# Kernel tuning notes

Measured on AMD Instinct MI355X. Metric: run time of the kernel, lower is better.

The kernel has to match this reference:

```python
import jax, jax.numpy as jnp
import numpy as np


def _dir_loss(sim, mask_f, ms):
    # sim: [N1, N2] similarities; mask_f: [N1, N2] float 0/1 positives; ms: [N1] float row-selection.
    # Row i contributes sum_{p in pos(i), n in neg(i)} -logsigmoid(sim[i,p] - sim[i,n])
    # = sum_{p,n} mp[i,p]*mn[i,n]*softplus(sim[i,n] - sim[i,p]).
    mp = mask_f * ms[:, None]           # [N1, N2] positive weights (zero for unselected rows)
    mn = (1.0 - mask_f) * ms[:, None]   # [N1, N2] negative weights
    # term[i, p, n] = softplus(sim[i, n] - sim[i, p]) = -logsigmoid(sim[i, p] - sim[i, n])
    term = jax.nn.softplus(sim[:, None, :] - sim[:, :, None])  # [N1, N2, N2]
    loss = jnp.sum(mp[:, :, None] * mn[:, None, :] * term)
    pair_num = jnp.sum(mp.sum(axis=1) * mn.sum(axis=1))
    return loss, pair_num


def setup_inputs() -> dict:
    key = jax.random.key(0)
    k1, k2, k3, k4, k5 = jax.random.split(key, 5)
    N1, N2, D = 512, 512, 1024
    return {
        "features1": jax.random.normal(k1, (N1, D), dtype=jnp.float32),
        "features2": jax.random.normal(k2, (N2, D), dtype=jnp.float32),
        "mask": jax.random.randint(k3, (N1, N2), 0, 2, dtype=jnp.int32),
        "mask_sents1": jax.random.randint(k4, (N1,), 0, 2).astype(jnp.bool_),
        "mask_sents2": jax.random.randint(k5, (N2,), 0, 2).astype(jnp.bool_),
    }


def reference(features1, features2, mask, mask_sents1, mask_sents2):
    # sim_type == 'dot' (default): raw dot-product similarity, no normalization,
    # and temperature is never applied in the original forward.
    dt = features1.dtype
    mask_f = mask.astype(dt)
    ms1 = mask_sents1.astype(dt)
    ms2 = mask_sents2.astype(dt)
    sim = features1 @ features2.T  # [N1, N2]
    loss1, pn1 = _dir_loss(sim, mask_f, ms1)
    loss2, pn2 = _dir_loss(sim.T, mask_f.T, ms2)
    loss = loss1 + loss2
    pair_num = pn1 + pn2
    return jnp.where(pair_num > 0, loss / pair_num, loss)
```

## Files before the change

kernel.cpp:

```cpp
#include <hip/hip_runtime.h>

#define NN 512
#define DD 1024

typedef __attribute__((ext_vector_type(8))) short short8;
typedef __attribute__((ext_vector_type(4))) float f32x4;

__device__ __forceinline__ float fast_exp2(float x) {
#if __has_builtin(__builtin_amdgcn_exp2f)
  return __builtin_amdgcn_exp2f(x);
#else
  return __expf(x * 0.6931471805599453f);
#endif
}
__device__ __forceinline__ float fast_log2(float x) {
#if __has_builtin(__builtin_amdgcn_logf)
  return __builtin_amdgcn_logf(x);
#else
  return __logf(x) * 1.4426950408889634f;
#endif
}

__device__ __forceinline__ void cvt2(float f0, float f1, unsigned& hi, unsigned& lo) {
  const unsigned u0 = __float_as_uint(f0), u1 = __float_as_uint(f1);
  const unsigned h0 = u0 & 0xFFFF0000u, h1 = u1 & 0xFFFF0000u;
  const float r0 = f0 - __uint_as_float(h0);
  const float r1 = f1 - __uint_as_float(h1);
  hi = (u0 >> 16) | h1;
  lo = (__float_as_uint(r0) >> 16) | (__float_as_uint(r1) & 0xFFFF0000u);
}

__device__ __forceinline__ void store8(unsigned short* hp, unsigned short* lp,
                                       float4 f0, float4 f1) {
  uint4 hi, lo;
  cvt2(f0.x, f0.y, hi.x, lo.x);
  cvt2(f0.z, f0.w, hi.y, lo.y);
  cvt2(f1.x, f1.y, hi.z, lo.z);
  cvt2(f1.z, f1.w, hi.w, lo.w);
  *(uint4*)hp = hi;
  *(uint4*)lp = lo;
}

__global__ __launch_bounds__(256) void gemm_kernel(const float* __restrict__ A,
                                                   const float* __restrict__ B,
                                                   float* __restrict__ simP,
                                                   float* __restrict__ simTP,
                                                   int ks) {
  __shared__ unsigned short Ah[64][40];
  __shared__ unsigned short Al[64][40];
  __shared__ unsigned short Bh[64][40];
  __shared__ unsigned short Bl[64][40];
  const int t = threadIdx.x;
  const int lane = t & 63;
  const int w = t >> 6;
  const int wm = w >> 1, wn = w & 1;
  const int row0 = blockIdx.y * 64, col0 = blockIdx.x * 64;
  const int z = blockIdx.z;
  const int kspan = DD / ks;
  const int kbeg = z * kspan;
  const int srow = t >> 2;
  const int skq = (t & 3) << 3;

  f32x4 acc[2][2] = {{{0.f, 0.f, 0.f, 0.f}, {0.f, 0.f, 0.f, 0.f}},
                     {{0.f, 0.f, 0.f, 0.f}, {0.f, 0.f, 0.f, 0.f}}};

  const int ksel = (lane >> 4) << 3;
  const int ar0 = wm * 32 + (lane & 15);
  const int br0 = wn * 32 + (lane & 15);

  for (int kb = 0; kb < kspan; kb += 32) {
    const float4 a0 = *(const float4*)&A[(row0 + srow) * DD + kbeg + kb + skq];
    const float4 a1 = *(const float4*)&A[(row0 + srow) * DD + kbeg + kb + skq + 4];
    const float4 b0 = *(const float4*)&B[(col0 + srow) * DD + kbeg + kb + skq];
    const float4 b1 = *(const float4*)&B[(col0 + srow) * DD + kbeg + kb + skq + 4];
    __syncthreads();
    store8(&Ah[srow][skq], &Al[srow][skq], a0, a1);
    store8(&Bh[srow][skq], &Bl[srow][skq], b0, b1);
    __syncthreads();
    short8 ah0 = *(const short8*)&Ah[ar0][ksel];
    short8 ah1 = *(const short8*)&Ah[ar0 + 16][ksel];
    short8 al0 = *(const short8*)&Al[ar0][ksel];
    short8 al1 = *(const short8*)&Al[ar0 + 16][ksel];
    short8 bh0 = *(const short8*)&Bh[br0][ksel];
    short8 bh1 = *(const short8*)&Bh[br0 + 16][ksel];
    short8 bl0 = *(const short8*)&Bl[br0][ksel];
    short8 bl1 = *(const short8*)&Bl[br0 + 16][ksel];
    acc[0][0] = __builtin_amdgcn_mfma_f32_16x16x32_bf16(ah0, bh0, acc[0][0], 0, 0, 0);
    acc[0][1] = __builtin_amdgcn_mfma_f32_16x16x32_bf16(ah0, bh1, acc[0][1], 0, 0, 0);
    acc[1][0] = __builtin_amdgcn_mfma_f32_16x16x32_bf16(ah1, bh0, acc[1][0], 0, 0, 0);
    acc[1][1] = __builtin_amdgcn_mfma_f32_16x16x32_bf16(ah1, bh1, acc[1][1], 0, 0, 0);
    acc[0][0] = __builtin_amdgcn_mfma_f32_16x16x32_bf16(ah0, bl0, acc[0][0], 0, 0, 0);
    acc[0][1] = __builtin_amdgcn_mfma_f32_16x16x32_bf16(ah0, bl1, acc[0][1], 0, 0, 0);
    acc[1][0] = __builtin_amdgcn_mfma_f32_16x16x32_bf16(ah1, bl0, acc[1][0], 0, 0, 0);
    acc[1][1] = __builtin_amdgcn_mfma_f32_16x16x32_bf16(ah1, bl1, acc[1][1], 0, 0, 0);
    acc[0][0] = __builtin_amdgcn_mfma_f32_16x16x32_bf16(al0, bh0, acc[0][0], 0, 0, 0);
    acc[0][1] = __builtin_amdgcn_mfma_f32_16x16x32_bf16(al0, bh1, acc[0][1], 0, 0, 0);
    acc[1][0] = __builtin_amdgcn_mfma_f32_16x16x32_bf16(al1, bh0, acc[1][0], 0, 0, 0);
    acc[1][1] = __builtin_amdgcn_mfma_f32_16x16x32_bf16(al1, bh1, acc[1][1], 0, 0, 0);
  }

  float* Cz = simP + (size_t)z * NN * NN;
  float* Tz = simTP + (size_t)z * NN * NN;
#pragma unroll
  for (int qm = 0; qm < 2; ++qm) {
    const int mb = row0 + wm * 32 + qm * 16 + ((lane >> 4) << 2);
#pragma unroll
    for (int qn = 0; qn < 2; ++qn) {
      const int n = col0 + wn * 32 + qn * 16 + (lane & 15);
#pragma unroll
      for (int r = 0; r < 4; ++r) Cz[(mb + r) * NN + n] = acc[qm][qn][r];
      *(f32x4*)&Tz[n * NN + mb] = acc[qm][qn];
    }
  }
}

template <int KS>
__global__ __launch_bounds__(512) void loss_kernel(const float* __restrict__ simP,
                                                   const float* __restrict__ simTP,
                                                   const int* __restrict__ mask,
                                                   const unsigned char* __restrict__ ms1,
                                                   const unsigned char* __restrict__ ms2,
                                                   float* __restrict__ lossB,
                                                   float* __restrict__ pairB) {
  __shared__ __align__(16) float posL[NN];
  __shared__ __align__(16) float negL[NN];
  __shared__ int wsum[8];
  __shared__ float wred[8];
  const int rd = blockIdx.x;
  const int dir = rd >> 9;
  const int idx = rd & (NN - 1);
  const int t = threadIdx.x;
  const int lane = t & 63;
  const int w = t >> 6;
  const unsigned char sel = dir ? ms2[idx] : ms1[idx];
  if (!sel) {
    if (t == 0) { lossB[rd] = 0.f; pairB[rd] = 0.f; }
    return;
  }
  float v = 0.f;
  int m;
  if (dir == 0) {
#pragma unroll
    for (int zz = 0; zz < KS; ++zz) v += simP[(size_t)zz * NN * NN + idx * NN + t];
    m = mask[idx * NN + t];
  } else {
#pragma unroll
    for (int zz = 0; zz < KS; ++zz) v += simTP[(size_t)zz * NN * NN + idx * NN + t];
    m = mask[t * NN + idx];
  }
  const unsigned long long bal = __ballot(m != 0);
  const unsigned long long lt = (1ull << lane) - 1ull;
  const int c = __popcll(bal & lt);
  const int tc = __popcll(bal);
  if (lane == 0) wsum[w] = tc;
  __syncthreads();
  int wp = 0, npos = 0;
#pragma unroll
  for (int q = 0; q < 8; ++q) {
    const int s = wsum[q];
    npos += s;
    if (q < w) wp += s;
  }
  const float LOG2E = 1.4426950408889634f;
  const int pos = wp + c;
  if (m) posL[pos] = v * LOG2E;
  else   negL[t - pos] = v * LOG2E;
  __syncthreads();

  const int nneg = NN - npos;
  const int sp = (npos >> 1) & ~3;
  const int ph = t & 1;
  const float* pp = &posL[ph ? sp : 0];
  const int cnt = (ph ? npos : sp) - (ph ? sp : 0);
  const int cnt4 = cnt & ~3;

  float sum = 0.f;
  for (int n = (t >> 1); n < nneg; n += 256) {
    const float yn = negL[n];
    float l0 = 0.f, l1 = 0.f, l2 = 0.f, l3 = 0.f;
    float p0 = 1.f, p1 = 1.f, p2 = 1.f, p3 = 1.f;
#pragma unroll 2
    for (int k = 0; k < cnt4; k += 4) {
      const float4 sq = *(const float4*)&pp[k];
      const float x0 = yn - sq.x; l0 += fmaxf(x0, 0.f); p0 = fmaf(p0, fast_exp2(-fabsf(x0)), p0);
      const float x1 = yn - sq.y; l1 += fmaxf(x1, 0.f); p1 = fmaf(p1, fast_exp2(-fabsf(x1)), p1);
      const float x2 = yn - sq.z; l2 += fmaxf(x2, 0.f); p2 = fmaf(p2, fast_exp2(-fabsf(x2)), p2);
      const float x3 = yn - sq.w; l3 += fmaxf(x3, 0.f); p3 = fmaf(p3, fast_exp2(-fabsf(x3)), p3);
    }
    for (int k = cnt4; k < cnt; ++k) {
      const float x = yn - pp[k];
      l0 += fmaxf(x, 0.f);
      p0 = fmaf(p0, fast_exp2(-fabsf(x)), p0);
    }
    sum += ((l0 + l1) + (l2 + l3)) +
           ((fast_log2(p0) + fast_log2(p1)) + (fast_log2(p2) + fast_log2(p3)));
  }
  sum *= 0.6931471805599453f;

  for (int off = 32; off > 0; off >>= 1) sum += __shfl_down(sum, off);
  if (lane == 0) wred[w] = sum;
  __syncthreads();
  if (t == 0) {
    float bs = 0.f;
#pragma unroll
    for (int q = 0; q < 8; ++q) bs += wred[q];
    lossB[rd] = bs;
    pairB[rd] = (float)npos * (float)(NN - npos);
  }
}

__global__ __launch_bounds__(256) void final_kernel(const float* __restrict__ lossB,
                                                    const float* __restrict__ pairB,
                                                    float* __restrict__ out) {
  __shared__ double rl[256];
  __shared__ double rp[256];
  const int t = threadIdx.x;
  double al = 0.0, ap = 0.0;
  for (int i = t; i < 1024; i += 256) { al += (double)lossB[i]; ap += (double)pairB[i]; }
  rl[t] = al; rp[t] = ap; __syncthreads();
  for (int st = 128; st > 0; st >>= 1) {
    if (t < st) { rl[t] += rl[t + st]; rp[t] += rp[t + st]; }
    __syncthreads();
  }
  if (t == 0) {
    const double pn = rp[0];
    out[0] = (float)((pn > 0.0) ? rl[0] / pn : rl[0]);
  }
}

extern "C" void kernel_launch(void* const* d_in, const int* in_sizes, int n_in,
                              void* d_out, int out_size, void* d_ws, size_t ws_size,
                              hipStream_t stream) {
  const float* f1 = (const float*)d_in[0];
  const float* f2 = (const float*)d_in[1];
  const int* mask = (const int*)d_in[2];
  const unsigned char* ms1 = (const unsigned char*)d_in[3];
  const unsigned char* ms2 = (const unsigned char*)d_in[4];
  float* out = (float*)d_out;

  auto need = [](int ks) -> size_t {
    return ((size_t)2 * ks * NN * NN + 1024u + 1024u) * sizeof(float);
  };
  const int ks = (ws_size >= need(8)) ? 8 : ((ws_size >= need(4)) ? 4 : 1);

  float* sim   = (float*)d_ws;
  float* simT  = sim + (size_t)ks * NN * NN;
  float* lossB = simT + (size_t)ks * NN * NN;
  float* pairB = lossB + 1024;

  gemm_kernel<<<dim3(8, 8, ks), 256, 0, stream>>>(f1, f2, sim, simT, ks);
  if (ks == 8) {
    loss_kernel<8><<<1024, 512, 0, stream>>>(sim, simT, mask, ms1, ms2, lossB, pairB);
  } else if (ks == 4) {
    loss_kernel<4><<<1024, 512, 0, stream>>>(sim, simT, mask, ms1, ms2, lossB, pairB);
  } else {
    loss_kernel<1><<<1024, 512, 0, stream>>>(sim, simT, mask, ms1, ms2, lossB, pairB);
  }
  final_kernel<<<1, 256, 0, stream>>>(lossB, pairB, out);
}
```

Measured before the change: 28.14 us.

## Fuse GEMM, loss and final reduction into one cooperative kernel with grid syncs

Replaces the three launches (split-K GEMM, per-row loss, final reduction) with a single cooperative kernel of 512 blocks that uses grid.sync between phases. The GEMM phase uses only half the threads per block, and each block then handles two loss rows (one per direction). The aim is to remove launch overhead and inter-kernel gaps. In exchange it adds grid barrier cost, leaves threads idle during the GEMM, and has lower parallelism in the loss phase than the 1024-block launch. It also checks occupancy before choosing this path.

```diff
diff --git a/kernel.cpp b/kernel.cpp
--- a/kernel.cpp
+++ b/kernel.cpp
@@ -1,4 +1,7 @@
 #include <hip/hip_runtime.h>
+#include <hip/hip_cooperative_groups.h>
+
+namespace cg = cooperative_groups;
 
 #define NN 512
 #define DD 1024
@@ -39,6 +42,213 @@
   cvt2(f1.z, f1.w, hi.w, lo.w);
   *(uint4*)hp = hi;
   *(uint4*)lp = lo;
+}
+
+template <int KS>
+__global__ __launch_bounds__(512, 4) void fused_kernel(const float* __restrict__ A,
+                                                       const float* __restrict__ B,
+                                                       const int* __restrict__ mask,
+                                                       const unsigned char* __restrict__ ms1,
+                                                       const unsigned char* __restrict__ ms2,
+                                                       float* __restrict__ simP,
+                                                       float* __restrict__ simTP,
+                                                       float* __restrict__ lossB,
+                                                       float* __restrict__ pairB,
+                                                       float* __restrict__ out) {
+  __shared__ unsigned short Ah[64][40];
+  __shared__ unsigned short Al[64][40];
+  __shared__ unsigned short Bh[64][40];
+  __shared__ unsigned short Bl[64][40];
+  __shared__ __align__(16) float posL[NN];
+  __shared__ __align__(16) float negL[NN];
+  __shared__ int wsum[8];
+  __shared__ float wred[8];
+  __shared__ double rfin[512];
+
+  cg::grid_group grid = cg::this_grid();
+  const int bid = blockIdx.x;
+  const int t = threadIdx.x;
+
+  {
+    const bool act = t < 256;
+    const int lane = t & 63;
+    const int w4 = t >> 6;
+    const int wm = w4 >> 1, wn = w4 & 1;
+    const int tx = bid & 7, ty = (bid >> 3) & 7, tz = bid >> 6;
+    const int row0 = ty * 64, col0 = tx * 64;
+    const int kspan = DD / KS;
+    const int kbeg = tz * kspan;
+    const int srow = t >> 2;
+    const int skq = (t & 3) << 3;
+
+    f32x4 acc[2][2] = {{{0.f, 0.f, 0.f, 0.f}, {0.f, 0.f, 0.f, 0.f}},
+                       {{0.f, 0.f, 0.f, 0.f}, {0.f, 0.f, 0.f, 0.f}}};
+    const int ksel = (lane >> 4) << 3;
+    const int ar0 = wm * 32 + (lane & 15);
+    const int br0 = wn * 32 + (lane & 15);
+
+    for (int kb = 0; kb < kspan; kb += 32) {
+      float4 a0, a1, b0, b1;
+      if (act) {
+        a0 = *(const float4*)&A[(row0 + srow) * DD + kbeg + kb + skq];
+        a1 = *(const float4*)&A[(row0 + srow) * DD + kbeg + kb + skq + 4];
+        b0 = *(const float4*)&B[(col0 + srow) * DD + kbeg + kb + skq];
+        b1 = *(const float4*)&B[(col0 + srow) * DD + kbeg + kb + skq + 4];
+      }
+      __syncthreads();
+      if (act) {
+        store8(&Ah[srow][skq], &Al[srow][skq], a0, a1);
+        store8(&Bh[srow][skq], &Bl[srow][skq], b0, b1);
+      }
+      __syncthreads();
+      if (act) {
+        short8 ah0 = *(const short8*)&Ah[ar0][ksel];
+        short8 ah1 = *(const short8*)&Ah[ar0 + 16][ksel];
+        short8 al0 = *(const short8*)&Al[ar0][ksel];
+        short8 al1 = *(const short8*)&Al[ar0 + 16][ksel];
+        short8 bh0 = *(const short8*)&Bh[br0][ksel];
+        short8 bh1 = *(const short8*)&Bh[br0 + 16][ksel];
+        short8 bl0 = *(const short8*)&Bl[br0][ksel];
+        short8 bl1 = *(const short8*)&Bl[br0 + 16][ksel];
+        acc[0][0] = __builtin_amdgcn_mfma_f32_16x16x32_bf16(ah0, bh0, acc[0][0], 0, 0, 0);
+        acc[0][1] = __builtin_amdgcn_mfma_f32_16x16x32_bf16(ah0, bh1, acc[0][1], 0, 0, 0);
+        acc[1][0] = __builtin_amdgcn_mfma_f32_16x16x32_bf16(ah1, bh0, acc[1][0], 0, 0, 0);
+        acc[1][1] = __builtin_amdgcn_mfma_f32_16x16x32_bf16(ah1, bh1, acc[1][1], 0, 0, 0);
+        acc[0][0] = __builtin_amdgcn_mfma_f32_16x16x32_bf16(ah0, bl0, acc[0][0], 0, 0, 0);
+        acc[0][1] = __builtin_amdgcn_mfma_f32_16x16x32_bf16(ah0, bl1, acc[0][1], 0, 0, 0);
+        acc[1][0] = __builtin_amdgcn_mfma_f32_16x16x32_bf16(ah1, bl0, acc[1][0], 0, 0, 0);
+        acc[1][1] = __builtin_amdgcn_mfma_f32_16x16x32_bf16(ah1, bl1, acc[1][1], 0, 0, 0);
+        acc[0][0] = __builtin_amdgcn_mfma_f32_16x16x32_bf16(al0, bh0, acc[0][0], 0, 0, 0);
+        acc[0][1] = __builtin_amdgcn_mfma_f32_16x16x32_bf16(al0, bh1, acc[0][1], 0, 0, 0);
+        acc[1][0] = __builtin_amdgcn_mfma_f32_16x16x32_bf16(al1, bh0, acc[1][0], 0, 0, 0);
+        acc[1][1] = __builtin_amdgcn_mfma_f32_16x16x32_bf16(al1, bh1, acc[1][1], 0, 0, 0);
+      }
+    }
+    if (act) {
+      float* Cz = simP + (size_t)tz * NN * NN;
+      float* Tz = simTP + (size_t)tz * NN * NN;
+#pragma unroll
+      for (int qm = 0; qm < 2; ++qm) {
+        const int mb = row0 + wm * 32 + qm * 16 + ((lane >> 4) << 2);
+#pragma unroll
+        for (int qn = 0; qn < 2; ++qn) {
+          const int n = col0 + wn * 32 + qn * 16 + (lane & 15);
+#pragma unroll
+          for (int r = 0; r < 4; ++r) Cz[(mb + r) * NN + n] = acc[qm][qn][r];
+          *(f32x4*)&Tz[n * NN + mb] = acc[qm][qn];
+        }
+      }
+    }
+  }
+
+  grid.sync();
+
+  for (int half = 0; half < 2; ++half) {
+    const int rd = bid + (half << 9);
+    const int dir = half;
+    const int idx = bid;
+    const int lane = t & 63;
+    const int w = t >> 6;
+    __syncthreads();
+    const unsigned char sel = dir ? ms2[idx] : ms1[idx];
+    if (!sel) {
+      if (t == 0) { lossB[rd] = 0.f; pairB[rd] = 0.f; }
+      continue;
+    }
+    float v = 0.f;
+    int m;
+    if (dir == 0) {
+#pragma unroll
+      for (int zz = 0; zz < KS; ++zz) v += simP[(size_t)zz * NN * NN + idx * NN + t];
+      m = mask[idx * NN + t];
+    } else {
+#pragma unroll
+      for (int zz = 0; zz < KS; ++zz) v += simTP[(size_t)zz * NN * NN + idx * NN + t];
+      m = mask[t * NN + idx];
+    }
+    const unsigned long long bal = __ballot(m != 0);
+    const unsigned long long ltm = (1ull << lane) - 1ull;
+    const int c = __popcll(bal & ltm);
+    const int tc = __popcll(bal);
+    if (lane == 0) wsum[w] = tc;
+    __syncthreads();
+    int wp = 0, npos = 0;
+#pragma unroll
+    for (int q = 0; q < 8; ++q) {
+      const int s = wsum[q];
+      npos += s;
+      if (q < w) wp += s;
+    }
+    const float LOG2E = 1.4426950408889634f;
+    const int pos = wp + c;
+    if (m) posL[pos] = v * LOG2E;
+    else   negL[t - pos] = v * LOG2E;
+    __syncthreads();
+
+    const int nneg = NN - npos;
+    const int sp = (npos >> 1) & ~3;
+    const int ph = t & 1;
+    const float* pp = &posL[ph ? sp : 0];
+    const int cnt = (ph ? npos : sp) - (ph ? sp : 0);
+    const int cnt4 = cnt & ~3;
+
+    float sum = 0.f;
+    for (int n = (t >> 1); n < nneg; n += 256) {
+      const float yn = negL[n];
+      float l0 = 0.f, l1 = 0.f, l2 = 0.f, l3 = 0.f;
+      float p0 = 1.f, p1 = 1.f, p2 = 1.f, p3 = 1.f;
+#pragma unroll 2
+      for (int k = 0; k < cnt4; k += 4) {
+        const float4 sq = *(const float4*)&pp[k];
+        const float x0 = yn - sq.x; l0 += fmaxf(x0, 0.f); p0 = fmaf(p0, fast_exp2(-fabsf(x0)), p0);
+        const float x1 = yn - sq.y; l1 += fmaxf(x1, 0.f); p1 = fmaf(p1, fast_exp2(-fabsf(x1)), p1);
+        const float x2 = yn - sq.z; l2 += fmaxf(x2, 0.f); p2 = fmaf(p2, fast_exp2(-fabsf(x2)), p2);
+        const float x3 = yn - sq.w; l3 += fmaxf(x3, 0.f); p3 = fmaf(p3, fast_exp2(-fabsf(x3)), p3);
+      }
+      for (int k = cnt4; k < cnt; ++k) {
+        const float x = yn - pp[k];
+        l0 += fmaxf(x, 0.f);
+        p0 = fmaf(p0, fast_exp2(-fabsf(x)), p0);
+      }
+      sum += ((l0 + l1) + (l2 + l3)) +
+             ((fast_log2(p0) + fast_log2(p1)) + (fast_log2(p2) + fast_log2(p3)));
+    }
+    sum *= 0.6931471805599453f;
+
+    for (int off = 32; off > 0; off >>= 1) sum += __shfl_down(sum, off);
+    if (lane == 0) wred[w] = sum;
+    __syncthreads();
+    if (t == 0) {
+      float bs = 0.f;
+#pragma unroll
+      for (int q = 0; q < 8; ++q) bs += wred[q];
+      lossB[rd] = bs;
+      pairB[rd] = (float)npos * (float)(NN - npos);
+    }
+  }
+
+  grid.sync();
+
+  if (bid == 0) {
+    double al = (double)lossB[t] + (double)lossB[t + 512];
+    double ap = (double)pairB[t] + (double)pairB[t + 512];
+    rfin[t] = al; __syncthreads();
+    for (int st = 256; st > 0; st >>= 1) {
+      if (t < st) rfin[t] += rfin[t + st];
+      __syncthreads();
+    }
+    const double ltot = rfin[0];
+    __syncthreads();
+    rfin[t] = ap; __syncthreads();
+    for (int st = 256; st > 0; st >>= 1) {
+      if (t < st) rfin[t] += rfin[t + st];
+      __syncthreads();
+    }
+    if (t == 0) {
+      const double pn = rfin[0];
+      out[0] = (float)((pn > 0.0) ? ltot / pn : ltot);
+    }
+  }
 }
 
 __global__ __launch_bounds__(256) void gemm_kernel(const float* __restrict__ A,
@@ -63,7 +273,6 @@
 
   f32x4 acc[2][2] = {{{0.f, 0.f, 0.f, 0.f}, {0.f, 0.f, 0.f, 0.f}},
                      {{0.f, 0.f, 0.f, 0.f}, {0.f, 0.f, 0.f, 0.f}}};
-
   const int ksel = (lane >> 4) << 3;
   const int ar0 = wm * 32 + (lane & 15);
   const int br0 = wn * 32 + (lane & 15);
@@ -149,8 +358,8 @@
     m = mask[t * NN + idx];
   }
   const unsigned long long bal = __ballot(m != 0);
-  const unsigned long long lt = (1ull << lane) - 1ull;
-  const int c = __popcll(bal & lt);
+  const unsigned long long ltm = (1ull << lane) - 1ull;
+  const int c = __popcll(bal & ltm);
   const int tc = __popcll(bal);
   if (lane == 0) wsum[w] = tc;
   __syncthreads();
@@ -248,13 +457,29 @@
   float* lossB = simT + (size_t)ks * NN * NN;
   float* pairB = lossB + 1024;
 
-  gemm_kernel<<<dim3(8, 8, ks), 256, 0, stream>>>(f1, f2, sim, simT, ks);
+  bool coop_ok = false;
   if (ks == 8) {
-    loss_kernel<8><<<1024, 512, 0, stream>>>(sim, simT, mask, ms1, ms2, lossB, pairB);
-  } else if (ks == 4) {
-    loss_kernel<4><<<1024, 512, 0, stream>>>(sim, simT, mask, ms1, ms2, lossB, pairB);
+    int nb = 0;
+    if (hipOccupancyMaxActiveBlocksPerMultiprocessor(&nb, fused_kernel<8>, 512, 0) ==
+            hipSuccess &&
+        nb >= 2) {
+      coop_ok = true;
+    }
+  }
+
+  if (coop_ok) {
+    void* args[] = {(void*)&f1, (void*)&f2, (void*)&mask, (void*)&ms1, (void*)&ms2,
+                    (void*)&sim, (void*)&simT, (void*)&lossB, (void*)&pairB, (void*)&out};
+    hipLaunchCooperativeKernel((void*)fused_kernel<8>, dim3(512), dim3(512), args, 0, stream);
   } else {
-    loss_kernel<1><<<1024, 512, 0, stream>>>(sim, simT, mask, ms1, ms2, lossB, pairB);
-  }
-  final_kernel<<<1, 256, 0, stream>>>(lossB, pairB, out);
-}
+    gemm_kernel<<<dim3(8, 8, ks), 256, 0, stream>>>(f1, f2, sim, simT, ks);
+    if (ks == 8) {
+      loss_kernel<8><<<1024, 512, 0, stream>>>(sim, simT, mask, ms1, ms2, lossB, pairB);
+    } else if (ks == 4) {
+      loss_kernel<4><<<1024, 512, 0, stream>>>(sim, simT, mask, ms1, ms2, lossB, pairB);
+    } else {
+      loss_kernel<1><<<1024, 512, 0, stream>>>(sim, simT, mask, ms1, ms2, lossB, pairB);
+    }
+    final_kernel<<<1, 256, 0, stream>>>(lossB, pairB, out);
+  }
+}
```

New measurement: 27.89 us. No clear change (-0.9%).
